# Performance work log

Hardware: AMD Instinct MI355X
Metric: run time of the kernel (lower is better)

## Reference

```python
import jax, jax.numpy as jnp
import numpy as np

VOCAB = 50257
DIM = 1024
GROUP = 128


def _sign_ste_fwd_only(x):
    s = jnp.sign(x)
    return jnp.where(s == 0, jnp.asarray(1.0, x.dtype), s)


def quantize_literati(w, scales, group_size=GROUP):
    # w: [V, D], scales: [V, D//G] (D divisible by G in this config)
    V, D = w.shape
    G = group_size
    w_groups = w.reshape(V, D // G, G)
    signs = _sign_ste_fwd_only(w_groups)
    s = jnp.maximum(scales, 1e-8)[..., None]  # clamp, [V, D//G, 1]
    return (signs * s).reshape(V, D)


def setup_inputs() -> dict:
    key = jax.random.key(0)
    k1, k2, k3 = jax.random.split(key, 3)
    input_ids = jax.random.randint(k1, (8, 2048), 0, VOCAB)
    weight = jax.random.normal(k2, (VOCAB, DIM), dtype=jnp.float32) * 0.02
    scales = jax.random.uniform(k3, (VOCAB, DIM // GROUP), dtype=jnp.float32) * 0.1 + 0.05
    return {"input_ids": input_ids, "weight": weight, "scales": scales}


def reference(input_ids, weight, scales):
    w_q = quantize_literati(weight, scales)  # [V, D]
    return jnp.take(w_q, input_ids, axis=0)  # [B, S, D]
```

## Files before the change

### kernel.cpp

```cpp
#include <hip/hip_runtime.h>
#include <stdint.h>

#define DIM 1024
#define GROUP 128
#define NGROUP (DIM / GROUP)

__global__ __launch_bounds__(256) void literati_embed_kernel(
    const int*   __restrict__ ids,
    const float* __restrict__ weight,
    const float* __restrict__ scales,
    float*       __restrict__ out,
    int n_tokens)
{
    const int token = blockIdx.x;
    if (token >= n_tokens) return;

    const int tid = threadIdx.x;
    const int row = ids[token];

    const float4* wrow = reinterpret_cast<const float4*>(weight + (size_t)row * DIM);
    float4*       orow = reinterpret_cast<float4*>(out + (size_t)token * DIM);

    float s = scales[row * NGROUP + (tid >> 5)];
    s = fmaxf(s, 1e-8f);
    const uint32_t sbits = __float_as_uint(s);

    const float4 w = wrow[tid];

    float4 r;
    {
        uint32_t b = sbits | ((w.x != 0.0f) ? (__float_as_uint(w.x) & 0x80000000u) : 0u);
        r.x = __uint_as_float(b);
    }
    {
        uint32_t b = sbits | ((w.y != 0.0f) ? (__float_as_uint(w.y) & 0x80000000u) : 0u);
        r.y = __uint_as_float(b);
    }
    {
        uint32_t b = sbits | ((w.z != 0.0f) ? (__float_as_uint(w.z) & 0x80000000u) : 0u);
        r.z = __uint_as_float(b);
    }
    {
        uint32_t b = sbits | ((w.w != 0.0f) ? (__float_as_uint(w.w) & 0x80000000u) : 0u);
        r.w = __uint_as_float(b);
    }

    orow[tid] = r;
}

extern "C" void kernel_launch(void* const* d_in, const int* in_sizes, int n_in,
                              void* d_out, int out_size, void* d_ws, size_t ws_size,
                              hipStream_t stream) {
    const int*   ids    = (const int*)d_in[0];
    const float* weight = (const float*)d_in[1];
    const float* scales = (const float*)d_in[2];
    float*       out    = (float*)d_out;

    const int n_tokens = in_sizes[0];

    literati_embed_kernel<<<n_tokens, 256, 0, stream>>>(ids, weight, scales, out, n_tokens);
}
```

Before: 274.2 us.

## Process eight tokens per block with batched loads and nontemporal stores

Each block now handles eight tokens: it first reads all eight ids, then issues all eight weight-row and scale loads before computing and writing, so more memory requests are in flight per thread. Output writes use nontemporal stores to avoid polluting cache with the streamed output. The grid shrinks eightfold, which lowers block-launch overhead but also cuts the number of wavefronts available to hide latency, and register use goes up.

```diff
diff --git a/kernel.cpp b/kernel.cpp
--- a/kernel.cpp
+++ b/kernel.cpp
@@ -4,6 +4,9 @@
 #define DIM 1024
 #define GROUP 128
 #define NGROUP (DIM / GROUP)
+#define TPB 8
+
+typedef float  fx4 __attribute__((ext_vector_type(4)));
 
 __global__ __launch_bounds__(256) void literati_embed_kernel(
     const int*   __restrict__ ids,
@@ -12,40 +15,43 @@
     float*       __restrict__ out,
     int n_tokens)
 {
-    const int token = blockIdx.x;
-    if (token >= n_tokens) return;
+    const int tid  = threadIdx.x;
+    const int gidx = tid >> 5;
+    const int step = gridDim.x * TPB;
 
-    const int tid = threadIdx.x;
-    const int row = ids[token];
+    for (int base = blockIdx.x * TPB; base < n_tokens; base += step) {
+        int rows[TPB];
+#pragma unroll
+        for (int i = 0; i < TPB; ++i) {
+            int t = base + i;
+            rows[i] = ids[t < n_tokens ? t : (n_tokens - 1)];
+        }
 
-    const float4* wrow = reinterpret_cast<const float4*>(weight + (size_t)row * DIM);
-    float4*       orow = reinterpret_cast<float4*>(out + (size_t)token * DIM);
+        fx4   w[TPB];
+        float s[TPB];
+#pragma unroll
+        for (int i = 0; i < TPB; ++i) {
+            w[i] = reinterpret_cast<const fx4*>(weight + (size_t)rows[i] * DIM)[tid];
+            s[i] = scales[rows[i] * NGROUP + gidx];
+        }
 
-    float s = scales[row * NGROUP + (tid >> 5)];
-    s = fmaxf(s, 1e-8f);
-    const uint32_t sbits = __float_as_uint(s);
-
-    const float4 w = wrow[tid];
-
-    float4 r;
-    {
-        uint32_t b = sbits | ((w.x != 0.0f) ? (__float_as_uint(w.x) & 0x80000000u) : 0u);
-        r.x = __uint_as_float(b);
+#pragma unroll
+        for (int i = 0; i < TPB; ++i) {
+            int t = base + i;
+            if (t < n_tokens) {
+                const uint32_t sb = __float_as_uint(fmaxf(s[i], 1e-8f));
+                fx4 r;
+#pragma unroll
+                for (int j = 0; j < 4; ++j) {
+                    float wj = w[i][j];
+                    uint32_t b = sb | ((wj != 0.0f) ? (__float_as_uint(wj) & 0x80000000u) : 0u);
+                    r[j] = __uint_as_float(b);
+                }
+                fx4* op = reinterpret_cast<fx4*>(out + (size_t)t * DIM) + tid;
+                __builtin_nontemporal_store(r, op);
+            }
+        }
     }
-    {
-        uint32_t b = sbits | ((w.y != 0.0f) ? (__float_as_uint(w.y) & 0x80000000u) : 0u);
-        r.y = __uint_as_float(b);
-    }
-    {
-        uint32_t b = sbits | ((w.z != 0.0f) ? (__float_as_uint(w.z) & 0x80000000u) : 0u);
-        r.z = __uint_as_float(b);
-    }
-    {
-        uint32_t b = sbits | ((w.w != 0.0f) ? (__float_as_uint(w.w) & 0x80000000u) : 0u);
-        r.w = __uint_as_float(b);
-    }
-
-    orow[tid] = r;
 }
 
 extern "C" void kernel_launch(void* const* d_in, const int* in_sizes, int n_in,
@@ -58,5 +64,7 @@
 
     const int n_tokens = in_sizes[0];
 
-    literati_embed_kernel<<<n_tokens, 256, 0, stream>>>(ids, weight, scales, out, n_tokens);
+    const int grid = (n_tokens + TPB - 1) / TPB;
+
+    literati_embed_kernel<<<grid, 256, 0, stream>>>(ids, weight, scales, out, n_tokens);
 }
```

Result: no change. 273.4 us (-0.3%).
